# Optimization experiments

Measured on AMD Instinct MI355X. Metric: run time of the kernel, lower is better.

The kernel has to match this reference:

```python
import jax, jax.numpy as jnp
import numpy as np

T, H, W_, CIN, LAT, HID, OUT, NHL = 32, 64, 64, 3, 256, 256, 3, 3
OMEGA = 30.0  # SIREN sine frequency


def _uniform(key, shape, fan_in):
    b = np.sqrt(6.0 / fan_in) / OMEGA
    return jax.random.uniform(key, shape, jnp.float32, -b, b)


def setup_inputs() -> dict:
    key = jax.random.key(0)
    ks = jax.random.split(key, 10)
    return {
        "coords": jax.random.normal(ks[0], (T, H, W_, CIN), jnp.float32),
        "latents": jax.random.normal(ks[1], (T, LAT), jnp.float32),
        # shared SIREN weights (nf_net): W stored as (out, in) like nn.Linear
        "W0": _uniform(ks[2], (HID, CIN), CIN),
        "b0": jnp.zeros((HID,), jnp.float32),
        "Wh": _uniform(ks[3], (NHL, HID, HID), HID),
        "bh": jnp.zeros((NHL, HID), jnp.float32),
        "Wf": _uniform(ks[4], (OUT, HID), HID),
        "bf": jnp.zeros((OUT,), jnp.float32),
        # hypernet weight generators (hw_net), no bias
        "HW0": _uniform(ks[5], (HID * CIN, LAT), LAT),
        "HWh": _uniform(ks[6], (NHL, HID * HID, LAT), LAT),
        # hypernet bias generators (hb_net), no bias
        "HB": _uniform(ks[7], (NHL + 1, HID, LAT), LAT),
    }


def reference(coords, latents, W0, b0, Wh, bh, Wf, bf, HW0, HWh, HB):
    t = latents.shape[0]
    # per-frame hyper biases for all layers: (t, NHL+1, HID)
    hb = jnp.einsum('tl,khl->tkh', latents, HB)
    # layer 0: per-frame weight (t, HID, CIN)
    hw0 = (latents @ HW0.T).reshape(t, HID, CIN)
    x = coords  # (t,h,w,CIN)
    x = (x @ W0.T + b0
         + jnp.einsum('thwi,toi->thwo', x, hw0)
         + hb[:, 0][:, None, None, :])
    x = jnp.sin(OMEGA * x)
    for i in range(NHL):
        hw = (latents @ HWh[i].T).reshape(t, HID, HID)  # (t, HID, HID)
        x = (x @ Wh[i].T + bh[i]
             + jnp.einsum('thwi,toi->thwo', x, hw)
             + hb[:, i + 1][:, None, None, :])
        x = jnp.sin(OMEGA * x)
    return x @ Wf.T + bf  # (t,h,w,OUT)
```

## Files before the change

### kernel.cpp

```cpp
#include <hip/hip_runtime.h>
#include <cstdint>
#include <cstddef>

typedef __attribute__((ext_vector_type(8))) _Float16 f16x8;
typedef __attribute__((ext_vector_type(2))) __fp16 h2;
typedef __attribute__((ext_vector_type(16))) float f32x16;

#define LO_SCALE 2048.0f
#define LO_INV   (1.0f / 2048.0f)
#define OMEGA_SC 4.774648292756860f

union H8 { f16x8 v; _Float16 h[8]; };
union HU { f16x8 v; h2 p[4]; };


__global__ __launch_bounds__(256) void kab(
    const float* __restrict__ latents, const float* __restrict__ W0,
    const float* __restrict__ b0, const float* __restrict__ bh,
    const float* __restrict__ HW0, const float* __restrict__ HB,
    const float* __restrict__ Wh, const float* __restrict__ HWh,
    _Float16* __restrict__ w0blob, float* __restrict__ beff,
    _Float16* __restrict__ whblob) {
  __shared__ float lat_t[8192];
  int tid = threadIdx.x, bid = blockIdx.x;

  if (bid >= 768) {
    int id = (bid - 768) * 256 + tid;
    if (id < 32768) {
      int t = id >> 10, rem = id & 1023;
      int r2 = rem & 127, part = r2 >> 6, lane = r2 & 63;
      int nf = rem >> 7;
      int o = nf * 32 + (lane & 31), kc = lane >> 5;
      const float* lat = latents + t * 256;
      H8 outv;
#pragma unroll
      for (int j = 0; j < 8; ++j) outv.h[j] = (_Float16)0.0f;
#pragma unroll
      for (int j = 0; j < 8; ++j) {
        int i = (j & 3) + 8 * (j >> 2) + 16 * kc;
        if (i < 3) {
          const float* row = HW0 + (o * 3 + i) * 256;
          float s = W0[o * 3 + i];
          for (int k = 0; k < 256; k += 4)
            s += row[k] * lat[k] + row[k + 1] * lat[k + 1] +
                 row[k + 2] * lat[k + 2] + row[k + 3] * lat[k + 3];
          s *= OMEGA_SC;
          _Float16 hi = (_Float16)s;
          outv.h[j] = part ? (_Float16)((s - (float)hi) * LO_SCALE) : hi;
        }
      }
      *(f16x8*)(w0blob + (size_t)id * 8) = outv.v;
    } else {
      int v = id - 32768;
      int t = v >> 10, k = (v >> 8) & 3, hm = v & 255;
      float base = (k == 0) ? b0[hm] : bh[(k - 1) * 256 + hm];
      const float* lat = latents + t * 256;
      const float* row = HB + (size_t)(k * 256 + hm) * 256;
      float s = base;
      for (int kk = 0; kk < 256; kk += 4)
        s += row[kk] * lat[kk] + row[kk + 1] * lat[kk + 1] +
             row[kk + 2] * lat[kk + 2] + row[kk + 3] * lat[kk + 3];
      beff[v] = s * OMEGA_SC;
    }
    return;
  }

  int h = bid & 1, ks = (bid >> 1) & 15, nf = (bid >> 5) & 7, l = bid >> 8;

  {
    int f = tid >> 3, kb = (tid & 7) * 32;
#pragma unroll
    for (int m = 0; m < 32; m += 4) {
      float4 v = *(const float4*)(latents + f * 256 + kb + m);
      lat_t[(kb + m + 0) * 32 + f] = v.x;
      lat_t[(kb + m + 1) * 32 + f] = v.y;
      lat_t[(kb + m + 2) * 32 + f] = v.z;
      lat_t[(kb + m + 3) * 32 + f] = v.w;
    }
  }
  __syncthreads();

  int oo = tid >> 3, jj = tid & 7;
  int o = nf * 32 + oo;
  int i = (ks >> 1) * 32 + (ks & 1) * 4 + (jj & 3) + 8 * ((jj >> 2) & 1) + 16 * h;
  int r = o * 256 + i;
  const float* rowp = HWh + ((size_t)l * 65536 + (size_t)r) * 256;

  float acc[32];
#pragma unroll
  for (int f = 0; f < 32; ++f) acc[f] = 0.f;

  float curf[16], nxtf[16];
#pragma unroll
  for (int q = 0; q < 4; ++q)
    *(float4*)(curf + q * 4) = *(const float4*)(rowp + q * 4);

  for (int kc = 0; kc < 16; ++kc) {
    if (kc < 15) {
#pragma unroll
      for (int q = 0; q < 4; ++q)
        *(float4*)(nxtf + q * 4) = *(const float4*)(rowp + (kc + 1) * 16 + q * 4);
    }
    const float* lp = lat_t + kc * 512;
#pragma unroll
    for (int m = 0; m < 16; ++m) {
      float hw = curf[m];
#pragma unroll
      for (int fq = 0; fq < 8; ++fq) {
        float4 lv = *(const float4*)(lp + m * 32 + fq * 4);
        acc[fq * 4 + 0] += hw * lv.x;
        acc[fq * 4 + 1] += hw * lv.y;
        acc[fq * 4 + 2] += hw * lv.z;
        acc[fq * 4 + 3] += hw * lv.w;
      }
    }
#pragma unroll
    for (int q = 0; q < 16; ++q) curf[q] = nxtf[q];
  }

  float whv = Wh[l * 65536 + r];
  size_t cbase = (size_t)(nf * 16 + ks) * 1024 + (size_t)h * 256 + (size_t)tid;
#pragma unroll
  for (int t = 0; t < 32; ++t) {
    float w = (acc[t] + whv) * OMEGA_SC;
    _Float16 hi = (_Float16)w;
    _Float16 lo = (_Float16)((w - (float)hi) * LO_SCALE);
    size_t b = (size_t)(t * 3 + l) * 131072 + cbase;
    whblob[b] = hi;
    whblob[b + 512] = lo;
  }
}

__global__ __launch_bounds__(256, 2) void kb_siren(
    const float* __restrict__ coords, const _Float16* __restrict__ whblob,
    const _Float16* __restrict__ w0blob, const float* __restrict__ beff,
    const float* __restrict__ Wf, const float* __restrict__ bf,
    float* __restrict__ out) {
  __shared__ _Float16 xs_hi[64 * 264];
  __shared__ _Float16 xs_lo[64 * 264];
  __shared__ float wf_s[768];
  __shared__ float red[768];
  int tid = threadIdx.x;
  int bid0 = blockIdx.x;
  int bid = (bid0 & 7) * 256 + (bid0 >> 3);
  int t = bid >> 6, tile = bid & 63;
  int wv = tid >> 6, lane = tid & 63, col = lane & 31, h = lane >> 5;

  if (tid < 192) {
    int c = tid >> 6;
    int pq = (tid & 63) * 4;
    int blk = pq >> 5, p32 = pq & 31, hq = p32 >> 4, rr = p32 & 15;
    int src = c * 256 + blk * 32 + 8 * (rr >> 2) + 4 * hq;
    *(float4*)(wf_s + tid * 4) = *(const float4*)(Wf + src);
  }
  if (tid < 64) {
    const float* cp = coords + (size_t)(t * 4096 + tile * 64 + tid) * 3;
    float c0 = cp[0], c1 = cp[1], c2 = cp[2];
    H8 hv, lv, z;
#pragma unroll
    for (int j = 0; j < 8; ++j) { hv.h[j] = (_Float16)0.f; lv.h[j] = (_Float16)0.f; z.h[j] = (_Float16)0.f; }
    _Float16 h0 = (_Float16)c0, h1 = (_Float16)c1, h2_ = (_Float16)c2;
    hv.h[0] = h0; hv.h[1] = h1; hv.h[2] = h2_;
    lv.h[0] = (_Float16)((c0 - (float)h0) * LO_SCALE);
    lv.h[1] = (_Float16)((c1 - (float)h1) * LO_SCALE);
    lv.h[2] = (_Float16)((c2 - (float)h2_) * LO_SCALE);
    *(f16x8*)(xs_hi + tid * 264) = hv.v;
    *(f16x8*)(xs_lo + tid * 264) = lv.v;
    *(f16x8*)(xs_hi + tid * 264 + 8) = z.v;
    *(f16x8*)(xs_lo + tid * 264 + 8) = z.v;
  }
  __syncthreads();

  f32x16 accA[2][2], accB[2][2];

  auto init_bias = [&](int bk) {
#pragma unroll
    for (int fr = 0; fr < 2; ++fr) {
      const float* bp = beff + ((t * 4 + bk) << 8) + (wv * 2 + fr) * 32 + h * 4;
#pragma unroll
      for (int rq = 0; rq < 4; ++rq) {
        float4 bvv = *(const float4*)(bp + rq * 8);
        float ba[4];
        *(float4*)ba = bvv;
#pragma unroll
        for (int q = 0; q < 4; ++q) {
          accA[fr][0][rq * 4 + q] = ba[q];
          accA[fr][1][rq * 4 + q] = ba[q];
          accB[fr][0][rq * 4 + q] = 0.f;
          accB[fr][1][rq * 4 + q] = 0.f;
        }
      }
    }
  };

  auto aload4 = [&](const _Float16* blobL, int NS, int ks,
                    f16x8& a0h, f16x8& a0l, f16x8& a1h, f16x8& a1l) {
    const _Float16* p0 = blobL + (size_t)(((wv * 2 + 0) * NS + ks) * 2) * 512 + lane * 8;
    const _Float16* p1 = blobL + (size_t)(((wv * 2 + 1) * NS + ks) * 2) * 512 + lane * 8;
    a0h = *(const f16x8*)p0;
    a0l = *(const f16x8*)(p0 + 512);
    a1h = *(const f16x8*)p1;
    a1l = *(const f16x8*)(p1 + 512);
  };

  auto bload = [&](int ks, f16x8& b0h, f16x8& b0l, f16x8& b1h, f16x8& b1l) {
    int off0 = col * 264 + ks * 16 + h * 8;
    int off1 = (32 + col) * 264 + ks * 16 + h * 8;
    b0h = *(const f16x8*)(xs_hi + off0);
    b0l = *(const f16x8*)(xs_lo + off0);
    b1h = *(const f16x8*)(xs_hi + off1);
    b1l = *(const f16x8*)(xs_lo + off1);
  };

  auto mfma12 = [&](f16x8 a0h, f16x8 a0l, f16x8 a1h, f16x8 a1l,
                    f16x8 b0h, f16x8 b0l, f16x8 b1h, f16x8 b1l) {
    __builtin_amdgcn_s_setprio(1);
    accA[0][0] = __builtin_amdgcn_mfma_f32_32x32x16_f16(a0h, b0h, accA[0][0], 0, 0, 0);
    accA[1][0] = __builtin_amdgcn_mfma_f32_32x32x16_f16(a1h, b0h, accA[1][0], 0, 0, 0);
    accA[0][1] = __builtin_amdgcn_mfma_f32_32x32x16_f16(a0h, b1h, accA[0][1], 0, 0, 0);
    accA[1][1] = __builtin_amdgcn_mfma_f32_32x32x16_f16(a1h, b1h, accA[1][1], 0, 0, 0);
    accB[0][0] = __builtin_amdgcn_mfma_f32_32x32x16_f16(a0h, b0l, accB[0][0], 0, 0, 0);
    accB[1][0] = __builtin_amdgcn_mfma_f32_32x32x16_f16(a1h, b0l, accB[1][0], 0, 0, 0);
    accB[0][1] = __builtin_amdgcn_mfma_f32_32x32x16_f16(a0h, b1l, accB[0][1], 0, 0, 0);
    accB[1][1] = __builtin_amdgcn_mfma_f32_32x32x16_f16(a1h, b1l, accB[1][1], 0, 0, 0);
    accB[0][0] = __builtin_amdgcn_mfma_f32_32x32x16_f16(a0l, b0h, accB[0][0], 0, 0, 0);
    accB[1][0] = __builtin_amdgcn_mfma_f32_32x32x16_f16(a1l, b0h, accB[1][0], 0, 0, 0);
    accB[0][1] = __builtin_amdgcn_mfma_f32_32x32x16_f16(a0l, b1h, accB[0][1], 0, 0, 0);
    accB[1][1] = __builtin_amdgcn_mfma_f32_32x32x16_f16(a1l, b1h, accB[1][1], 0, 0, 0);
    __builtin_amdgcn_s_setprio(0);
  };

  auto sin2pi = [](float x) {
    float f, r;
    asm("v_fract_f32 %0, %1" : "=v"(f) : "v"(x));
    asm("v_sin_f32 %0, %1" : "=v"(r) : "v"(f));
    return r;
  };

  auto epilogue = [&]() {
#pragma unroll
    for (int fr = 0; fr < 2; ++fr)
#pragma unroll
      for (int pf = 0; pf < 2; ++pf)
#pragma unroll
        for (int r = 0; r < 16; ++r)
          accA[fr][pf][r] = sin2pi(fmaf(accB[fr][pf][r], LO_INV, accA[fr][pf][r]));
    __syncthreads();
#pragma unroll
    for (int fr = 0; fr < 2; ++fr)
#pragma unroll
      for (int pf = 0; pf < 2; ++pf) {
        HU h0, h1, l0, l1;
#pragma unroll
        for (int q = 0; q < 4; ++q) {
          float va = accA[fr][pf][2 * q], vb = accA[fr][pf][2 * q + 1];
          h2 hp = __builtin_amdgcn_cvt_pkrtz(va, vb);
          h0.p[q] = hp;
          l0.p[q] = __builtin_amdgcn_cvt_pkrtz((va - (float)hp[0]) * LO_SCALE,
                                               (vb - (float)hp[1]) * LO_SCALE);
          float vc = accA[fr][pf][8 + 2 * q], vd = accA[fr][pf][8 + 2 * q + 1];
          h2 hq_ = __builtin_amdgcn_cvt_pkrtz(vc, vd);
          h1.p[q] = hq_;
          l1.p[q] = __builtin_amdgcn_cvt_pkrtz((vc - (float)hq_[0]) * LO_SCALE,
                                               (vd - (float)hq_[1]) * LO_SCALE);
        }
        int off = (pf * 32 + col) * 264 + wv * 64 + fr * 32 + h * 16;
        *(f16x8*)(xs_hi + off) = h0.v;
        *(f16x8*)(xs_hi + off + 8) = h1.v;
        *(f16x8*)(xs_lo + off) = l0.v;
        *(f16x8*)(xs_lo + off + 8) = l1.v;
      }
    __syncthreads();
  };

  const _Float16* bl0 = whblob + (size_t)(t * 3) * 131072;
  f16x8 c0h, c0l, c1h, c1l, n0h, n0l, n1h, n1l;
  f16x8 cb0h, cb0l, cb1h, cb1l, nb0h, nb0l, nb1h, nb1l;

  init_bias(0);
  aload4(w0blob + (size_t)t * 8192, 1, 0, c0h, c0l, c1h, c1l);
  bload(0, cb0h, cb0l, cb1h, cb1l);
  mfma12(c0h, c0l, c1h, c1l, cb0h, cb0l, cb1h, cb1l);
  aload4(bl0, 16, 0, c0h, c0l, c1h, c1l);
  epilogue();

#pragma unroll
  for (int li = 0; li < 3; ++li) {
    init_bias(li + 1);
    const _Float16* bl = whblob + (size_t)(t * 3 + li) * 131072;
    const _Float16* bln = whblob + (size_t)(t * 3 + li + 1) * 131072;
    bload(0, cb0h, cb0l, cb1h, cb1l);
#pragma unroll
    for (int ks2 = 0; ks2 < 8; ++ks2) {
      int ksB = ks2 * 2 + 1;
      bload(ksB, nb0h, nb0l, nb1h, nb1l);
      aload4(bl, 16, ksB, n0h, n0l, n1h, n1l);
      mfma12(c0h, c0l, c1h, c1l, cb0h, cb0l, cb1h, cb1l);
      if (ksB < 15) {
        bload(ksB + 1, cb0h, cb0l, cb1h, cb1l);
        aload4(bl, 16, ksB + 1, c0h, c0l, c1h, c1l);
      } else if (li < 2) {
        aload4(bln, 16, 0, c0h, c0l, c1h, c1l);
      }
      mfma12(n0h, n0l, n1h, n1l, nb0h, nb0l, nb1h, nb1l);
    }
    epilogue();
  }

  {
    float pc0 = 0.f, pc1 = 0.f, pc2 = 0.f;
    int px = tid & 63, kq = tid >> 6;
#pragma unroll
    for (int cc = 0; cc < 8; ++cc) {
      int k0 = kq * 64 + cc * 8;
      H8 hv, lv;
      hv.v = *(const f16x8*)(xs_hi + px * 264 + k0);
      lv.v = *(const f16x8*)(xs_lo + px * 264 + k0);
#pragma unroll
      for (int j = 0; j < 8; ++j) {
        float xv = (float)hv.h[j] + (float)lv.h[j] * LO_INV;
        pc0 += xv * wf_s[k0 + j];
        pc1 += xv * wf_s[256 + k0 + j];
        pc2 += xv * wf_s[512 + k0 + j];
      }
    }
    red[kq * 192 + px * 3 + 0] = pc0;
    red[kq * 192 + px * 3 + 1] = pc1;
    red[kq * 192 + px * 3 + 2] = pc2;
    __syncthreads();
    if (tid < 192) {
      int p2 = tid / 3, c = tid - p2 * 3;
      float s = bf[c];
#pragma unroll
      for (int q = 0; q < 4; ++q) s += red[q * 192 + p2 * 3 + c];
      out[(size_t)(t * 4096 + tile * 64 + p2) * 3 + c] = s;
    }
  }
}

extern "C" void kernel_launch(void* const* d_in, const int* in_sizes, int n_in,
                              void* d_out, int out_size, void* d_ws, size_t ws_size,
                              hipStream_t stream) {
  const float* coords  = (const float*)d_in[0];
  const float* latents = (const float*)d_in[1];
  const float* W0      = (const float*)d_in[2];
  const float* b0      = (const float*)d_in[3];
  const float* Wh      = (const float*)d_in[4];
  const float* bh      = (const float*)d_in[5];
  const float* Wf      = (const float*)d_in[6];
  const float* bf      = (const float*)d_in[7];
  const float* HW0     = (const float*)d_in[8];
  const float* HWh     = (const float*)d_in[9];
  const float* HB      = (const float*)d_in[10];
  float* outp = (float*)d_out;

  char* w = (char*)d_ws;
  _Float16* whblob = (_Float16*)w;
  _Float16* w0blob = (_Float16*)(w + 25165824);
  float*    beff   = (float*)(w + 25690112);

  kab<<<1024, 256, 0, stream>>>(latents, W0, b0, bh, HW0, HB, Wh, HWh,
                                w0blob, beff, whblob);
  kb_siren<<<2048, 256, 0, stream>>>(coords, whblob, w0blob, beff, Wf, bf, outp);
}
```

Before: 231.3 us.

## Deepen global A-fragment prefetch to three stages and use lighter LDS barriers

Restructures the hidden-layer MFMA loop so per-frame weight fragments are prefetched from global memory three k-steps ahead in a rotating buffer, and LDS B-fragments two steps ahead, replacing the previous two-stage ping-pong. The first three slices of each next layer are preloaded across the epilogue. Barriers in the epilogue become a plain lgkmcnt wait plus s_barrier rather than __syncthreads, so outstanding global loads are not forced to drain. Register pressure rises from the extra prefetch set, which could reduce occupancy or cause spills.

```diff
diff --git a/kernel.cpp b/kernel.cpp
--- a/kernel.cpp
+++ b/kernel.cpp
@@ -171,6 +171,11 @@
   }
   __syncthreads();
 
+  auto bar_lds = [] {
+    asm volatile("s_waitcnt lgkmcnt(0)" ::: "memory");
+    __builtin_amdgcn_s_barrier();
+  };
+
   f32x16 accA[2][2], accB[2][2];
 
   auto init_bias = [&](int bk) {
@@ -193,40 +198,41 @@
     }
   };
 
-  auto aload4 = [&](const _Float16* blobL, int NS, int ks,
-                    f16x8& a0h, f16x8& a0l, f16x8& a1h, f16x8& a1l) {
+  struct ASet { f16x8 a0h, a0l, a1h, a1l; };
+  struct BSet { f16x8 b0h, b0l, b1h, b1l; };
+
+  auto aload = [&](const _Float16* blobL, int NS, int ks, ASet& s) {
     const _Float16* p0 = blobL + (size_t)(((wv * 2 + 0) * NS + ks) * 2) * 512 + lane * 8;
     const _Float16* p1 = blobL + (size_t)(((wv * 2 + 1) * NS + ks) * 2) * 512 + lane * 8;
-    a0h = *(const f16x8*)p0;
-    a0l = *(const f16x8*)(p0 + 512);
-    a1h = *(const f16x8*)p1;
-    a1l = *(const f16x8*)(p1 + 512);
-  };
-
-  auto bload = [&](int ks, f16x8& b0h, f16x8& b0l, f16x8& b1h, f16x8& b1l) {
+    s.a0h = *(const f16x8*)p0;
+    s.a0l = *(const f16x8*)(p0 + 512);
+    s.a1h = *(const f16x8*)p1;
+    s.a1l = *(const f16x8*)(p1 + 512);
+  };
+
+  auto bload = [&](int ks, BSet& s) {
     int off0 = col * 264 + ks * 16 + h * 8;
-    int off1 = (32 + col) * 264 + ks * 16 + h * 8;
-    b0h = *(const f16x8*)(xs_hi + off0);
-    b0l = *(const f16x8*)(xs_lo + off0);
-    b1h = *(const f16x8*)(xs_hi + off1);
-    b1l = *(const f16x8*)(xs_lo + off1);
-  };
-
-  auto mfma12 = [&](f16x8 a0h, f16x8 a0l, f16x8 a1h, f16x8 a1l,
-                    f16x8 b0h, f16x8 b0l, f16x8 b1h, f16x8 b1l) {
+    int off1 = off0 + 32 * 264;
+    s.b0h = *(const f16x8*)(xs_hi + off0);
+    s.b0l = *(const f16x8*)(xs_lo + off0);
+    s.b1h = *(const f16x8*)(xs_hi + off1);
+    s.b1l = *(const f16x8*)(xs_lo + off1);
+  };
+
+  auto mfma12 = [&](const ASet& a, const BSet& b) {
     __builtin_amdgcn_s_setprio(1);
-    accA[0][0] = __builtin_amdgcn_mfma_f32_32x32x16_f16(a0h, b0h, accA[0][0], 0, 0, 0);
-    accA[1][0] = __builtin_amdgcn_mfma_f32_32x32x16_f16(a1h, b0h, accA[1][0], 0, 0, 0);
-    accA[0][1] = __builtin_amdgcn_mfma_f32_32x32x16_f16(a0h, b1h, accA[0][1], 0, 0, 0);
-    accA[1][1] = __builtin_amdgcn_mfma_f32_32x32x16_f16(a1h, b1h, accA[1][1], 0, 0, 0);
-    accB[0][0] = __builtin_amdgcn_mfma_f32_32x32x16_f16(a0h, b0l, accB[0][0], 0, 0, 0);
-    accB[1][0] = __builtin_amdgcn_mfma_f32_32x32x16_f16(a1h, b0l, accB[1][0], 0, 0, 0);
-    accB[0][1] = __builtin_amdgcn_mfma_f32_32x32x16_f16(a0h, b1l, accB[0][1], 0, 0, 0);
-    accB[1][1] = __builtin_amdgcn_mfma_f32_32x32x16_f16(a1h, b1l, accB[1][1], 0, 0, 0);
-    accB[0][0] = __builtin_amdgcn_mfma_f32_32x32x16_f16(a0l, b0h, accB[0][0], 0, 0, 0);
-    accB[1][0] = __builtin_amdgcn_mfma_f32_32x32x16_f16(a1l, b0h, accB[1][0], 0, 0, 0);
-    accB[0][1] = __builtin_amdgcn_mfma_f32_32x32x16_f16(a0l, b1h, accB[0][1], 0, 0, 0);
-    accB[1][1] = __builtin_amdgcn_mfma_f32_32x32x16_f16(a1l, b1h, accB[1][1], 0, 0, 0);
+    accA[0][0] = __builtin_amdgcn_mfma_f32_32x32x16_f16(a.a0h, b.b0h, accA[0][0], 0, 0, 0);
+    accA[1][0] = __builtin_amdgcn_mfma_f32_32x32x16_f16(a.a1h, b.b0h, accA[1][0], 0, 0, 0);
+    accA[0][1] = __builtin_amdgcn_mfma_f32_32x32x16_f16(a.a0h, b.b1h, accA[0][1], 0, 0, 0);
+    accA[1][1] = __builtin_amdgcn_mfma_f32_32x32x16_f16(a.a1h, b.b1h, accA[1][1], 0, 0, 0);
+    accB[0][0] = __builtin_amdgcn_mfma_f32_32x32x16_f16(a.a0h, b.b0l, accB[0][0], 0, 0, 0);
+    accB[1][0] = __builtin_amdgcn_mfma_f32_32x32x16_f16(a.a1h, b.b0l, accB[1][0], 0, 0, 0);
+    accB[0][1] = __builtin_amdgcn_mfma_f32_32x32x16_f16(a.a0h, b.b1l, accB[0][1], 0, 0, 0);
+    accB[1][1] = __builtin_amdgcn_mfma_f32_32x32x16_f16(a.a1h, b.b1l, accB[1][1], 0, 0, 0);
+    accB[0][0] = __builtin_amdgcn_mfma_f32_32x32x16_f16(a.a0l, b.b0h, accB[0][0], 0, 0, 0);
+    accB[1][0] = __builtin_amdgcn_mfma_f32_32x32x16_f16(a.a1l, b.b0h, accB[1][0], 0, 0, 0);
+    accB[0][1] = __builtin_amdgcn_mfma_f32_32x32x16_f16(a.a0l, b.b1h, accB[0][1], 0, 0, 0);
+    accB[1][1] = __builtin_amdgcn_mfma_f32_32x32x16_f16(a.a1l, b.b1h, accB[1][1], 0, 0, 0);
     __builtin_amdgcn_s_setprio(0);
   };
 
@@ -245,7 +251,7 @@
 #pragma unroll
         for (int r = 0; r < 16; ++r)
           accA[fr][pf][r] = sin2pi(fmaf(accB[fr][pf][r], LO_INV, accA[fr][pf][r]));
-    __syncthreads();
+    bar_lds();
 #pragma unroll
     for (int fr = 0; fr < 2; ++fr)
 #pragma unroll
@@ -270,18 +276,20 @@
         *(f16x8*)(xs_lo + off) = l0.v;
         *(f16x8*)(xs_lo + off + 8) = l1.v;
       }
-    __syncthreads();
-  };
-
-  const _Float16* bl0 = whblob + (size_t)(t * 3) * 131072;
-  f16x8 c0h, c0l, c1h, c1l, n0h, n0l, n1h, n1l;
-  f16x8 cb0h, cb0l, cb1h, cb1l, nb0h, nb0l, nb1h, nb1l;
+    bar_lds();
+  };
+
+  const _Float16* L0 = whblob + (size_t)(t * 3) * 131072;
+  ASet A[3];
+  BSet Bv[2];
 
   init_bias(0);
-  aload4(w0blob + (size_t)t * 8192, 1, 0, c0h, c0l, c1h, c1l);
-  bload(0, cb0h, cb0l, cb1h, cb1l);
-  mfma12(c0h, c0l, c1h, c1l, cb0h, cb0l, cb1h, cb1l);
-  aload4(bl0, 16, 0, c0h, c0l, c1h, c1l);
+  aload(w0blob + (size_t)t * 8192, 1, 0, A[0]);
+  bload(0, Bv[0]);
+  mfma12(A[0], Bv[0]);
+  aload(L0, 16, 0, A[0]);
+  aload(L0, 16, 1, A[1]);
+  aload(L0, 16, 2, A[2]);
   epilogue();
 
 #pragma unroll
@@ -289,20 +297,17 @@
     init_bias(li + 1);
     const _Float16* bl = whblob + (size_t)(t * 3 + li) * 131072;
     const _Float16* bln = whblob + (size_t)(t * 3 + li + 1) * 131072;
-    bload(0, cb0h, cb0l, cb1h, cb1l);
-#pragma unroll
-    for (int ks2 = 0; ks2 < 8; ++ks2) {
-      int ksB = ks2 * 2 + 1;
-      bload(ksB, nb0h, nb0l, nb1h, nb1l);
-      aload4(bl, 16, ksB, n0h, n0l, n1h, n1l);
-      mfma12(c0h, c0l, c1h, c1l, cb0h, cb0l, cb1h, cb1l);
-      if (ksB < 15) {
-        bload(ksB + 1, cb0h, cb0l, cb1h, cb1l);
-        aload4(bl, 16, ksB + 1, c0h, c0l, c1h, c1l);
+    bload(0, Bv[0]);
+    bload(1, Bv[1]);
+#pragma unroll
+    for (int ks = 0; ks < 16; ++ks) {
+      mfma12(A[(ks + li) % 3], Bv[ks & 1]);
+      if (ks + 3 < 16) {
+        aload(bl, 16, ks + 3, A[(ks + li) % 3]);
       } else if (li < 2) {
-        aload4(bln, 16, 0, c0h, c0l, c1h, c1l);
-      }
-      mfma12(n0h, n0l, n1h, n1l, nb0h, nb0l, nb1h, nb1l);
+        aload(bln, 16, ks - 13, A[(ks + li) % 3]);
+      }
+      if (ks + 2 < 16) bload(ks + 2, Bv[ks & 1]);
     }
     epilogue();
   }
```

Result: faster. 213.1 us (-7.9%).
